# Kernel tuning notes

Hardware: AMD Instinct MI355X
Metric: run time of the kernel (lower is better)

The kernel has to match this reference:

```python
import jax, jax.numpy as jnp
import numpy as np

NUM_HEADS = 16


def setup_inputs() -> dict:
    key = jax.random.key(0)
    ks = jax.random.split(key, 6)
    B, N, L, C = 2, 1024, 4096, 1024
    x_obj = jax.random.normal(ks[0], (B, N, C), dtype=jnp.float32)
    x_ctx = jax.random.normal(ks[1], (B, L, C), dtype=jnp.float32)
    s = 1.0 / np.sqrt(C)
    Wq = jax.random.normal(ks[2], (C, C), dtype=jnp.float32) * s
    Wkv = jax.random.normal(ks[3], (C, 2 * C), dtype=jnp.float32) * s
    Wproj = jax.random.normal(ks[4], (C, C), dtype=jnp.float32) * s
    bproj = jax.random.normal(ks[5], (C,), dtype=jnp.float32) * 0.01
    return {"x_obj": x_obj, "x_ctx": x_ctx, "Wq": Wq, "Wkv": Wkv,
            "Wproj": Wproj, "bproj": bproj}


def _split_heads(t, H):
    # [B, T, C] -> [B, H, T, d]
    B, T, C = t.shape
    return t.reshape(B, T, H, C // H).transpose(0, 2, 1, 3)


def reference(x_obj, x_ctx, Wq, Wkv, Wproj, bproj):
    B, N, C = x_obj.shape
    H = NUM_HEADS
    d = C // H
    scale = d ** -0.5

    q = _split_heads(x_obj @ Wq, H)                      # [B,H,N,d]

    kv_o = x_obj @ Wkv                                   # [B,N,2C] -> (2,H,d) split
    k_obj = _split_heads(kv_o[..., :C], H)               # [B,H,N,d]
    v_obj = _split_heads(kv_o[..., C:], H)

    kv_c = x_ctx @ Wkv                                   # [B,L,2C]
    k_ctx = _split_heads(kv_c[..., :C], H)               # [B,H,L,d]
    v_ctx = _split_heads(kv_c[..., C:], H)

    k = jnp.concatenate([k_obj, k_ctx], axis=2)          # [B,H,N+L,d]
    v = jnp.concatenate([v_obj, v_ctx], axis=2)

    attn = jnp.einsum('bhnd,bhmd->bhnm', q, k) * scale   # [B,H,N,N+L]
    attn = jax.nn.softmax(attn, axis=-1)
    out = jnp.einsum('bhnm,bhmd->bhnd', attn, v)         # [B,H,N,d]
    out = out.transpose(0, 2, 1, 3).reshape(B, N, C)
    return out @ Wproj + bproj
```

## Files before the change

### kernel.cpp

```cpp
#include <hip/hip_runtime.h>
#include <stdint.h>

typedef unsigned short u16;
typedef unsigned int   u32;
typedef __attribute__((ext_vector_type(8))) short bf16x8;
typedef __attribute__((ext_vector_type(4))) float f32x4;

__device__ __forceinline__ u16 f2bf(float f) {
    union { float f; u32 u; } v; v.f = f;
    return (u16)((v.u + 0x7FFFu + ((v.u >> 16) & 1u)) >> 16);
}
__device__ __forceinline__ float bf2f(u16 h) {
    union { u32 u; float f; } v; v.u = ((u32)h) << 16; return v.f;
}
__device__ __forceinline__ u32 fbits(float f) {
    union { float f; u32 u; } v; v.f = f; return v.u;
}

__device__ __forceinline__ void async16(const u16* g, u16* l) {
    typedef __attribute__((address_space(1))) const u32 gq;
    typedef __attribute__((address_space(3))) u32 lq;
    __builtin_amdgcn_global_load_lds((gq*)g, (lq*)l, 16, 0, 0);
}

__global__ void cvt_all_k(const float* __restrict__ xo, const float* __restrict__ xc,
                          u16* __restrict__ Xc,
                          const float* __restrict__ Wq, const float* __restrict__ Wkv,
                          const float* __restrict__ Wp,
                          u16* __restrict__ Wqt, u16* __restrict__ Wkt,
                          u16* __restrict__ Wpt)
{
    __shared__ __align__(16) u16 Ts[64][72];
    int id = blockIdx.x, t = threadIdx.x;
    if (id < 10240) {
        int row = id, cid = t * 4;
        int b = row >= 5120, s = row - b * 5120;
        const float* src = (s < 1024)
            ? xo + ((size_t)(b * 1024 + s)) * 1024 + cid
            : xc + ((size_t)(b * 4096 + s - 1024)) * 1024 + cid;
        float4 f = *(const float4*)src;
        union { u16 a[4]; uint2 v; } p;
        p.a[0]=f2bf(f.x); p.a[1]=f2bf(f.y); p.a[2]=f2bf(f.z); p.a[3]=f2bf(f.w);
        *(uint2*)(Xc + (size_t)row * 1024 + cid) = p.v;
        return;
    }
    int wid = id - 10240;
    const float* W; u16* Wt; int N, tile;
    if (wid < 256)      { W = Wq;  Wt = Wqt; N = 1024; tile = wid; }
    else if (wid < 768) { W = Wkv; Wt = Wkt; N = 2048; tile = wid - 256; }
    else                { W = Wp;  Wt = Wpt; N = 1024; tile = wid - 768; }
    int nt = N >> 6;
    int n0 = (tile % nt) * 64, k0 = (tile / nt) * 64;
    int lr = t >> 2, lc = (t & 3) * 16;
    const float* src = W + (size_t)(k0 + lr) * N + n0 + lc;
    union { u16 a[8]; uint4 v; } p0, p1;
    float4 f0 = *(const float4*)(src),      f1 = *(const float4*)(src + 4);
    float4 f2 = *(const float4*)(src + 8),  f3 = *(const float4*)(src + 12);
    p0.a[0]=f2bf(f0.x); p0.a[1]=f2bf(f0.y); p0.a[2]=f2bf(f0.z); p0.a[3]=f2bf(f0.w);
    p0.a[4]=f2bf(f1.x); p0.a[5]=f2bf(f1.y); p0.a[6]=f2bf(f1.z); p0.a[7]=f2bf(f1.w);
    p1.a[0]=f2bf(f2.x); p1.a[1]=f2bf(f2.y); p1.a[2]=f2bf(f2.z); p1.a[3]=f2bf(f2.w);
    p1.a[4]=f2bf(f3.x); p1.a[5]=f2bf(f3.y); p1.a[6]=f2bf(f3.z); p1.a[7]=f2bf(f3.w);
    *(uint4*)&Ts[lr][lc]     = p0.v;
    *(uint4*)&Ts[lr][lc + 8] = p1.v;
    __syncthreads();
    union { u16 a[8]; uint4 v; } q0, q1;
#pragma unroll
    for (int j = 0; j < 8; ++j) q0.a[j] = Ts[lc + j][lr];
#pragma unroll
    for (int j = 0; j < 8; ++j) q1.a[j] = Ts[lc + 8 + j][lr];
    u16* dst = Wt + (size_t)(n0 + lr) * 1024 + k0 + lc;
    *(uint4*)dst       = q0.v;
    *(uint4*)(dst + 8) = q1.v;
}

__global__ __launch_bounds__(256, 2)
void gemm_qkv(const u16* __restrict__ A, const u16* __restrict__ Wqt,
              const u16* __restrict__ Wkt, u16* __restrict__ q,
              u16* __restrict__ Kh, u16* __restrict__ Vh)
{
    __shared__ __align__(16) u16 smem[17408];
    u16* As = smem;
    u16* Bs = smem + 4096;

    const int t = threadIdx.x, w = t >> 6;
    const int lane = t & 63, quad = lane >> 4, l16 = lane & 15;
    const int id = blockIdx.x;
    const bool qm = id >= 1280;
    int m0, n0; const u16* Bt;
    if (qm) { int t2 = id - 1280; m0 = (t2 >> 3) * 128; n0 = (t2 & 7) * 128; Bt = Wqt; }
    else    { m0 = (id >> 4) * 128; n0 = (id & 15) * 128; Bt = Wkt; }
    const int wr = (w >> 1) * 64, wc = (w & 1) * 64;

    const int sr0 = w * 32 + (lane >> 2), sr1 = sr0 + 16;
    const int cg  = (lane & 3) ^ ((lane >> 4) & 3);
    u16* abase = As + w * 1024;
    u16* bbase = Bs + w * 1024;

    const u16 *ar0, *ar1;
    {
        int g0 = m0 + sr0, g1 = m0 + sr1;
        if (qm) {
            ar0 = A + ((size_t)(g0 >> 10) * 5120 + (g0 & 1023)) * 1024;
            ar1 = A + ((size_t)(g1 >> 10) * 5120 + (g1 & 1023)) * 1024;
        } else {
            ar0 = A + (size_t)g0 * 1024;
            ar1 = A + (size_t)g1 * 1024;
        }
        ar0 += cg * 8; ar1 += cg * 8;
    }
    const u16* br0 = Bt + (size_t)(n0 + sr0) * 1024 + cg * 8;
    const u16* br1 = Bt + (size_t)(n0 + sr1) * 1024 + cg * 8;

    f32x4 acc[4][4] = {};
    const int sel = (quad ^ (l16 >> 2)) * 8;

    for (int k0 = 0; k0 < 1024; k0 += 32) {
        async16(ar0 + k0, abase);
        async16(ar1 + k0, abase + 512);
        async16(br0 + k0, bbase);
        async16(br1 + k0, bbase + 512);
        __syncthreads();

        bf16x8 av[4], bv[4];
#pragma unroll
        for (int i = 0; i < 4; ++i)
            av[i] = *(const bf16x8*)&As[(wr + i * 16 + l16) * 32 + sel];
#pragma unroll
        for (int j = 0; j < 4; ++j)
            bv[j] = *(const bf16x8*)&Bs[(wc + j * 16 + l16) * 32 + sel];
#pragma unroll
        for (int i = 0; i < 4; ++i)
#pragma unroll
            for (int j = 0; j < 4; ++j)
                acc[i][j] = __builtin_amdgcn_mfma_f32_16x16x32_bf16(av[i], bv[j], acc[i][j], 0, 0, 0);
        __syncthreads();
    }

    if (qm) {
        const float SC = 0.180336880f;
#pragma unroll
        for (int j = 0; j < 4; ++j) {
            int col = n0 + wc + j * 16 + l16;
#pragma unroll
            for (int i = 0; i < 4; ++i) {
                int rowb = m0 + wr + i * 16 + quad * 4;
#pragma unroll
                for (int r = 0; r < 4; ++r)
                    q[(size_t)(rowb + r) * 1024 + col] = f2bf(acc[i][j][r] * SC);
            }
        }
        return;
    }
    int b = m0 >= 5120;
    int keyb = m0 - b * 5120;
    if (n0 < 1024) {
#pragma unroll
        for (int j = 0; j < 4; ++j) {
            int col = n0 + wc + j * 16 + l16;
#pragma unroll
            for (int i = 0; i < 4; ++i) {
                int rowb = m0 + wr + i * 16 + quad * 4;
                int key = rowb - b * 5120;
                int bh = b * 16 + (col >> 6), d = col & 63;
                u16* dst = Kh + ((size_t)bh * 5120 + key) * 64 + d;
#pragma unroll
                for (int r = 0; r < 4; ++r) dst[r * 64] = f2bf(acc[i][j][r]);
            }
        }
    } else {
        u16* T = smem;
#pragma unroll
        for (int j = 0; j < 4; ++j) {
            int d2 = wc + j * 16 + l16;
#pragma unroll
            for (int i = 0; i < 4; ++i) {
                int kl = wr + i * 16 + quad * 4;
                union { u16 a[4]; uint2 v; } pk;
#pragma unroll
                for (int r = 0; r < 4; ++r) pk.a[r] = f2bf(acc[i][j][r]);
                *(uint2*)&T[d2 * 136 + kl] = pk.v;
            }
        }
        __syncthreads();
        int hb = (n0 - 1024) >> 6;
#pragma unroll
        for (int p = 0; p < 8; ++p) {
            int idx = p * 256 + t;
            int d2 = idx >> 4, k0c = (idx & 15) * 8;
            uint4 vv = *(const uint4*)&T[d2 * 136 + k0c];
            int bh = b * 16 + hb + (d2 >> 6), d = d2 & 63;
            *(uint4*)(Vh + ((size_t)bh * 64 + d) * 5120 + keyb + k0c) = vv;
        }
    }
}

__global__ __launch_bounds__(256, 2)
void gemm_proj(const u16* __restrict__ A, const u16* __restrict__ Bt,
               const float* __restrict__ bias, float* __restrict__ Cf)
{
    __shared__ __align__(16) u16 As[128 * 32];
    __shared__ __align__(16) u16 Bs[64 * 32];

    const int t = threadIdx.x, w = t >> 6;
    const int lane = t & 63, quad = lane >> 4, l16 = lane & 15;
    const int m0 = blockIdx.y * 128, n0 = blockIdx.x * 64;
    const int wr = w * 32;

    const int sr0 = w * 32 + (lane >> 2), sr1 = sr0 + 16;
    const int cg  = (lane & 3) ^ ((lane >> 4) & 3);
    u16* abase = As + w * 1024;
    u16* bbase = Bs + w * 512;

    const u16* ar0 = A + (size_t)(m0 + sr0) * 1024 + cg * 8;
    const u16* ar1 = A + (size_t)(m0 + sr1) * 1024 + cg * 8;
    const u16* br0 = Bt + (size_t)(n0 + w * 16 + (lane >> 2)) * 1024 + cg * 8;

    f32x4 acc[2][4] = {};
    const int sel = (quad ^ (l16 >> 2)) * 8;

    for (int k0 = 0; k0 < 1024; k0 += 32) {
        async16(ar0 + k0, abase);
        async16(ar1 + k0, abase + 512);
        async16(br0 + k0, bbase);
        __syncthreads();

        bf16x8 av[2], bv[4];
#pragma unroll
        for (int i = 0; i < 2; ++i)
            av[i] = *(const bf16x8*)&As[(wr + i * 16 + l16) * 32 + sel];
#pragma unroll
        for (int j = 0; j < 4; ++j)
            bv[j] = *(const bf16x8*)&Bs[(j * 16 + l16) * 32 + sel];
#pragma unroll
        for (int i = 0; i < 2; ++i)
#pragma unroll
            for (int j = 0; j < 4; ++j)
                acc[i][j] = __builtin_amdgcn_mfma_f32_16x16x32_bf16(av[i], bv[j], acc[i][j], 0, 0, 0);
        __syncthreads();
    }

#pragma unroll
    for (int j = 0; j < 4; ++j) {
        int col = n0 + j * 16 + l16;
        float bvl = bias[col];
#pragma unroll
        for (int i = 0; i < 2; ++i) {
            int rowb = m0 + wr + i * 16 + quad * 4;
#pragma unroll
            for (int r = 0; r < 4; ++r)
                Cf[(size_t)(rowb + r) * 1024 + col] = acc[i][j][r] + bvl;
        }
    }
}

__global__ __launch_bounds__(256, 4)
void attn_k(const u16* __restrict__ Q, const u16* __restrict__ Kh,
            const u16* __restrict__ Vh, u16* __restrict__ Op,
            float* __restrict__ Lp)
{
    __shared__ __align__(16) u16 Ks[2][4096];
    __shared__ __align__(16) u16 Vt[2][4096];
    __shared__ __align__(16) u16 Ps[4096];

    const int tid  = threadIdx.x;
    const int wave = tid >> 6, lane = tid & 63;
    const int quad = lane >> 4, l16 = lane & 15;
    const int bx = blockIdx.x;
    const int x   = bx & 7;
    const int seq = bx >> 3;
    const int qt  = seq & 7;
    const int kg  = seq >> 3;
    const int g   = x + 8 * kg;
    const int part = g >> 5;
    const int bh   = g & 31;
    const int h = bh & 15, b = bh >> 4;

    const int qrow0 = b * 1024 + qt * 128 + wave * 32;
    const u16* qbase = Q + (size_t)qrow0 * 1024 + h * 64;

    bf16x8 aq[2][2];
#pragma unroll
    for (int rt = 0; rt < 2; ++rt) {
        aq[rt][0] = *(const bf16x8*)(qbase + (size_t)(rt * 16 + l16) * 1024 +      quad * 8);
        aq[rt][1] = *(const bf16x8*)(qbase + (size_t)(rt * 16 + l16) * 1024 + 32 + quad * 8);
    }

    union { u32 u[4]; bf16x8 v; } onesf;
#pragma unroll
    for (int i = 0; i < 4; ++i) onesf.u[i] = 0x3F803F80u;

    f32x4 o[2][4] = {};
    f32x4 lacc[2] = {};

    const u16* kbase = Kh + (size_t)bh * 5120 * 64;
    const u16* vbase = Vh + (size_t)bh * 64 * 5120;
    const int l7 = l16 & 7;
    u16* psw = Ps + wave * 1024;
    const int m_beg = part * 1280;

    const int r1 = tid >> 3;
    const int sl = tid & 7;
    const int xs = sl ^ (r1 & 7);
    const u16* kga = kbase + (size_t)(m_beg + 2 * r1) * 64 + xs * 8;
    const u16* vga = vbase + (size_t)r1 * 5120 + m_beg + xs * 8;
    u16* kldsw = &Ks[0][0] + wave * 512;
    u16* vldsw = &Vt[0][0] + wave * 512;

    async16(kga,              kldsw);
    async16(kga + 64,         kldsw + 2048);
    async16(vga,              vldsw);
    async16(vga + 32 * 5120,  vldsw + 2048);

    for (int c = 0; c < 20; ++c) {
        __syncthreads();

        if (c < 19) {
            const int nb = (c + 1) & 1;
            const u16* ka = kga + (size_t)(c + 1) * 4096;
            const u16* va = vga + (c + 1) * 64;
            u16* kd = &Ks[nb][0] + wave * 512;
            u16* vd = &Vt[nb][0] + wave * 512;
            async16(ka,             kd);
            async16(ka + 64,        kd + 2048);
            async16(va,             vd);
            async16(va + 32 * 5120, vd + 2048);
        }

        const u16* KsC = &Ks[c & 1][0];
        const u16* VtC = &Vt[c & 1][0];

        f32x4 s[2][4] = {};
        __builtin_amdgcn_s_setprio(1);
#pragma unroll
        for (int nt = 0; nt < 4; ++nt) {
            const u16* krow = KsC + (nt * 16 + l16) * 64;
            bf16x8 kb0 = *(const bf16x8*)(krow + ((quad     ^ l7) * 8));
            bf16x8 kb1 = *(const bf16x8*)(krow + (((4+quad) ^ l7) * 8));
#pragma unroll
            for (int rt = 0; rt < 2; ++rt) {
                s[rt][nt] = __builtin_amdgcn_mfma_f32_16x16x32_bf16(aq[rt][0], kb0, s[rt][nt], 0, 0, 0);
                s[rt][nt] = __builtin_amdgcn_mfma_f32_16x16x32_bf16(aq[rt][1], kb1, s[rt][nt], 0, 0, 0);
            }
        }
        __builtin_amdgcn_s_setprio(0);

#pragma unroll
        for (int rt = 0; rt < 2; ++rt) {
#pragma unroll
            for (int r = 0; r < 4; ++r) {
                float e0 = exp2f(s[rt][0][r]);
                float e1 = exp2f(s[rt][1][r]);
                float e2 = exp2f(s[rt][2][r]);
                float e3 = exp2f(s[rt][3][r]);
                u32 pwx = __builtin_amdgcn_perm(fbits(e2), fbits(e0), 0x07060302u);
                u32 pwy = __builtin_amdgcn_perm(fbits(e3), fbits(e1), 0x07060302u);
                int qr = quad * 4 + r;
                u16* prow = psw + qr * 64;
                *(u32*)(prow + ((( (l16 >> 2)    ) ^ (qr & 7)) * 8) + (l16 & 3) * 2) = pwx;
                *(u32*)(prow + ((( (l16 >> 2) + 4) ^ (qr & 7)) * 8) + (l16 & 3) * 2) = pwy;
            }

            asm volatile("s_waitcnt lgkmcnt(0)" ::: "memory");

            const u16* prow = psw + l16 * 64;
            bf16x8 pf0 = *(const bf16x8*)(prow + ((quad     ^ l7) * 8));
            bf16x8 pf1 = *(const bf16x8*)(prow + (((4+quad) ^ l7) * 8));

            __builtin_amdgcn_s_setprio(1);
            lacc[rt] = __builtin_amdgcn_mfma_f32_16x16x32_bf16(pf0, onesf.v, lacc[rt], 0, 0, 0);
            lacc[rt] = __builtin_amdgcn_mfma_f32_16x16x32_bf16(pf1, onesf.v, lacc[rt], 0, 0, 0);
#pragma unroll
            for (int dt = 0; dt < 4; ++dt) {
                const u16* vrow = VtC + (dt * 16 + l16) * 64;
                bf16x8 v0 = *(const bf16x8*)(vrow + ((quad     ^ l7) * 8));
                bf16x8 v1 = *(const bf16x8*)(vrow + (((4+quad) ^ l7) * 8));
                o[rt][dt] = __builtin_amdgcn_mfma_f32_16x16x32_bf16(pf0, v0, o[rt][dt], 0, 0, 0);
                o[rt][dt] = __builtin_amdgcn_mfma_f32_16x16x32_bf16(pf1, v1, o[rt][dt], 0, 0, 0);
            }
            __builtin_amdgcn_s_setprio(0);
        }
    }

    const int Rb = bh * 1024 + qt * 128 + wave * 32;
    u16* obase = Op + ((size_t)part << 21);
#pragma unroll
    for (int rt = 0; rt < 2; ++rt)
#pragma unroll
        for (int dt = 0; dt < 4; ++dt)
#pragma unroll
            for (int r = 0; r < 4; ++r) {
                int R = Rb + rt * 16 + quad * 4 + r;
                obase[(size_t)R * 64 + dt * 16 + l16] = f2bf(o[rt][dt][r]);
            }
    if (l16 == 0) {
#pragma unroll
        for (int rt = 0; rt < 2; ++rt)
#pragma unroll
            for (int r = 0; r < 4; ++r)
                Lp[part * 32768 + Rb + rt * 16 + quad * 4 + r] = lacc[rt][r];
    }
}

__global__ void comb_k(const u16* __restrict__ Op, const float* __restrict__ Lp,
                       u16* __restrict__ ao)
{
    int t = blockIdx.x * 256 + threadIdx.x;
    int R = t >> 4, dg = (t & 15) * 4;
    float l = Lp[R] + Lp[32768 + R] + Lp[65536 + R] + Lp[98304 + R];
    float a[4] = {0.f, 0.f, 0.f, 0.f};
#pragma unroll
    for (int p = 0; p < 4; ++p) {
        union { u16 a[4]; uint2 v; } w;
        w.v = *(const uint2*)(Op + ((size_t)p << 21) + (size_t)R * 64 + dg);
#pragma unroll
        for (int j = 0; j < 4; ++j) a[j] += bf2f(w.a[j]);
    }
    float inv = 1.f / l;
    int bh = R >> 10, n = R & 1023, b = bh >> 4, h = bh & 15;
    union { u16 a[4]; uint2 v; } out;
#pragma unroll
    for (int j = 0; j < 4; ++j) out.a[j] = f2bf(a[j] * inv);
    *(uint2*)(ao + (size_t)(b * 1024 + n) * 1024 + h * 64 + dg) = out.v;
}

extern "C" void kernel_launch(void* const* d_in, const int* in_sizes, int n_in,
                              void* d_out, int out_size, void* d_ws, size_t ws_size,
                              hipStream_t stream)
{
    const float* x_obj = (const float*)d_in[0];
    const float* x_ctx = (const float*)d_in[1];
    const float* Wq    = (const float*)d_in[2];
    const float* Wkv   = (const float*)d_in[3];
    const float* Wproj = (const float*)d_in[4];
    const float* bproj = (const float*)d_in[5];
    float* out = (float*)d_out;

    u16* Xc  = (u16*)d_ws;
    u16* ao  = Xc;
    u16* Op  = Xc + (size_t)2097152;
    u16* Wqt = Xc  + (size_t)10485760;
    u16* Wkt = Wqt + (size_t)1048576;
    u16* Wpt = Wkt + (size_t)2097152;
    u16* q   = Wpt + (size_t)1048576;
    u16* Kh  = q   + (size_t)2097152;
    u16* Vh  = Kh  + (size_t)10485760;
    float* Lp = (float*)(Wkt + (size_t)1048576);

    dim3 blk(256);
    cvt_all_k<<<dim3(11264), blk, 0, stream>>>(x_obj, x_ctx, Xc,
                                               Wq, Wkv, Wproj, Wqt, Wkt, Wpt);
    gemm_qkv<<<dim3(1408), blk, 0, stream>>>(Xc, Wqt, Wkt, q, Kh, Vh);
    attn_k<<<dim3(1024), blk, 0, stream>>>(q, Kh, Vh, Op, Lp);
    comb_k<<<dim3(2048), blk, 0, stream>>>(Op, Lp, ao);
    gemm_proj<<<dim3(16, 16), blk, 0, stream>>>(ao, Wpt, bproj, out);
}
```

Before: 244.4 us.

## Hoist V fragments, software-pipeline P tiles, and stagger block start with sleeps

The inner attention loop now loads the V fragments once per chunk and shares them across both row tiles, where before they were reloaded for each row tile. The exponentials for the second row tile are computed while the first tile's P is staged through LDS, so exp work overlaps LDS traffic. The goal is to cut redundant LDS reads and hide latency between the exp and MFMA phases. It also adds a per-block s_sleep delay based on block index to stagger block start times. That spreads out contention at launch but inserts idle cycles, and the hoisted V fragments raise register pressure.

```diff
diff --git a/kernel.cpp b/kernel.cpp
--- a/kernel.cpp
+++ b/kernel.cpp
@@ -275,6 +275,14 @@
     const int bh   = g & 31;
     const int h = bh & 15, b = bh >> 4;
 
+    {
+        int ph = (bx >> 8) & 3;
+        for (int i = 0; i < ph; ++i) {
+            __builtin_amdgcn_s_sleep(8);
+            __builtin_amdgcn_s_sleep(8);
+        }
+    }
+
     const int qrow0 = b * 1024 + qt * 128 + wave * 32;
     const u16* qbase = Q + (size_t)qrow0 * 1024 + h * 64;
 
@@ -344,41 +352,77 @@
         }
         __builtin_amdgcn_s_setprio(0);
 
-#pragma unroll
-        for (int rt = 0; rt < 2; ++rt) {
-#pragma unroll
-            for (int r = 0; r < 4; ++r) {
-                float e0 = exp2f(s[rt][0][r]);
-                float e1 = exp2f(s[rt][1][r]);
-                float e2 = exp2f(s[rt][2][r]);
-                float e3 = exp2f(s[rt][3][r]);
-                u32 pwx = __builtin_amdgcn_perm(fbits(e2), fbits(e0), 0x07060302u);
-                u32 pwy = __builtin_amdgcn_perm(fbits(e3), fbits(e1), 0x07060302u);
-                int qr = quad * 4 + r;
-                u16* prow = psw + qr * 64;
-                *(u32*)(prow + ((( (l16 >> 2)    ) ^ (qr & 7)) * 8) + (l16 & 3) * 2) = pwx;
-                *(u32*)(prow + ((( (l16 >> 2) + 4) ^ (qr & 7)) * 8) + (l16 & 3) * 2) = pwy;
-            }
-
-            asm volatile("s_waitcnt lgkmcnt(0)" ::: "memory");
-
-            const u16* prow = psw + l16 * 64;
-            bf16x8 pf0 = *(const bf16x8*)(prow + ((quad     ^ l7) * 8));
-            bf16x8 pf1 = *(const bf16x8*)(prow + (((4+quad) ^ l7) * 8));
-
-            __builtin_amdgcn_s_setprio(1);
-            lacc[rt] = __builtin_amdgcn_mfma_f32_16x16x32_bf16(pf0, onesf.v, lacc[rt], 0, 0, 0);
-            lacc[rt] = __builtin_amdgcn_mfma_f32_16x16x32_bf16(pf1, onesf.v, lacc[rt], 0, 0, 0);
-#pragma unroll
-            for (int dt = 0; dt < 4; ++dt) {
-                const u16* vrow = VtC + (dt * 16 + l16) * 64;
-                bf16x8 v0 = *(const bf16x8*)(vrow + ((quad     ^ l7) * 8));
-                bf16x8 v1 = *(const bf16x8*)(vrow + (((4+quad) ^ l7) * 8));
-                o[rt][dt] = __builtin_amdgcn_mfma_f32_16x16x32_bf16(pf0, v0, o[rt][dt], 0, 0, 0);
-                o[rt][dt] = __builtin_amdgcn_mfma_f32_16x16x32_bf16(pf1, v1, o[rt][dt], 0, 0, 0);
-            }
-            __builtin_amdgcn_s_setprio(0);
-        }
+        bf16x8 vf0[4], vf1[4];
+#pragma unroll
+        for (int dt = 0; dt < 4; ++dt) {
+            const u16* vrow = VtC + (dt * 16 + l16) * 64;
+            vf0[dt] = *(const bf16x8*)(vrow + ((quad     ^ l7) * 8));
+            vf1[dt] = *(const bf16x8*)(vrow + (((4+quad) ^ l7) * 8));
+        }
+
+#pragma unroll
+        for (int r = 0; r < 4; ++r) {
+            float e0 = exp2f(s[0][0][r]);
+            float e1 = exp2f(s[0][1][r]);
+            float e2 = exp2f(s[0][2][r]);
+            float e3 = exp2f(s[0][3][r]);
+            u32 pwx = __builtin_amdgcn_perm(fbits(e2), fbits(e0), 0x07060302u);
+            u32 pwy = __builtin_amdgcn_perm(fbits(e3), fbits(e1), 0x07060302u);
+            int qr = quad * 4 + r;
+            u16* prow = psw + qr * 64;
+            *(u32*)(prow + ((( (l16 >> 2)    ) ^ (qr & 7)) * 8) + (l16 & 3) * 2) = pwx;
+            *(u32*)(prow + ((( (l16 >> 2) + 4) ^ (qr & 7)) * 8) + (l16 & 3) * 2) = pwy;
+        }
+
+        u32 pw1[4][2];
+#pragma unroll
+        for (int r = 0; r < 4; ++r) {
+            float e0 = exp2f(s[1][0][r]);
+            float e1 = exp2f(s[1][1][r]);
+            float e2 = exp2f(s[1][2][r]);
+            float e3 = exp2f(s[1][3][r]);
+            pw1[r][0] = __builtin_amdgcn_perm(fbits(e2), fbits(e0), 0x07060302u);
+            pw1[r][1] = __builtin_amdgcn_perm(fbits(e3), fbits(e1), 0x07060302u);
+        }
+
+        asm volatile("s_waitcnt lgkmcnt(0)" ::: "memory");
+
+        const u16* prow = psw + l16 * 64;
+        bf16x8 pf0a = *(const bf16x8*)(prow + ((quad     ^ l7) * 8));
+        bf16x8 pf0b = *(const bf16x8*)(prow + (((4+quad) ^ l7) * 8));
+
+#pragma unroll
+        for (int r = 0; r < 4; ++r) {
+            int qr = quad * 4 + r;
+            u16* prw = psw + qr * 64;
+            *(u32*)(prw + ((( (l16 >> 2)    ) ^ (qr & 7)) * 8) + (l16 & 3) * 2) = pw1[r][0];
+            *(u32*)(prw + ((( (l16 >> 2) + 4) ^ (qr & 7)) * 8) + (l16 & 3) * 2) = pw1[r][1];
+        }
+
+        __builtin_amdgcn_s_setprio(1);
+        lacc[0] = __builtin_amdgcn_mfma_f32_16x16x32_bf16(pf0a, onesf.v, lacc[0], 0, 0, 0);
+        lacc[0] = __builtin_amdgcn_mfma_f32_16x16x32_bf16(pf0b, onesf.v, lacc[0], 0, 0, 0);
+#pragma unroll
+        for (int dt = 0; dt < 4; ++dt) {
+            o[0][dt] = __builtin_amdgcn_mfma_f32_16x16x32_bf16(pf0a, vf0[dt], o[0][dt], 0, 0, 0);
+            o[0][dt] = __builtin_amdgcn_mfma_f32_16x16x32_bf16(pf0b, vf1[dt], o[0][dt], 0, 0, 0);
+        }
+        __builtin_amdgcn_s_setprio(0);
+
+        asm volatile("s_waitcnt lgkmcnt(0)" ::: "memory");
+
+        bf16x8 pf1a = *(const bf16x8*)(prow + ((quad     ^ l7) * 8));
+        bf16x8 pf1b = *(const bf16x8*)(prow + (((4+quad) ^ l7) * 8));
+
+        __builtin_amdgcn_s_setprio(1);
+        lacc[1] = __builtin_amdgcn_mfma_f32_16x16x32_bf16(pf1a, onesf.v, lacc[1], 0, 0, 0);
+        lacc[1] = __builtin_amdgcn_mfma_f32_16x16x32_bf16(pf1b, onesf.v, lacc[1], 0, 0, 0);
+#pragma unroll
+        for (int dt = 0; dt < 4; ++dt) {
+            o[1][dt] = __builtin_amdgcn_mfma_f32_16x16x32_bf16(pf1a, vf0[dt], o[1][dt], 0, 0, 0);
+            o[1][dt] = __builtin_amdgcn_mfma_f32_16x16x32_bf16(pf1b, vf1[dt], o[1][dt], 0, 0, 0);
+        }
+        __builtin_amdgcn_s_setprio(0);
     }
 
     const int Rb = bh * 1024 + qt * 128 + wave * 32;
```

After: 270.4 us. 10.7% more time.

## Keep softmax probabilities in registers by transposing QK MFMA and permuting V

Applied to the files above, without the earlier changes.

The QK^T MFMA operands are swapped so the score fragment comes out transposed. Each lane can then pack its exp values straight into the A-operand layout for the PV MFMA, which removes the per-wave LDS round trip for P, its waitcnt stall and the Ps shared buffer. To match the new column order, V is loaded through registers with a permuted key offset and written into LDS itself, replacing the async global-to-LDS copy. K rows are now loaded contiguously instead of interleaved. The cost is more VGPR pressure and register-staged V loads that the asynchronous copy path no longer hides.

```diff
diff --git a/kernel.cpp b/kernel.cpp
--- a/kernel.cpp
+++ b/kernel.cpp
@@ -260,7 +260,6 @@
 {
     __shared__ __align__(16) u16 Ks[2][4096];
     __shared__ __align__(16) u16 Vt[2][4096];
-    __shared__ __align__(16) u16 Ps[4096];
 
     const int tid  = threadIdx.x;
     const int wave = tid >> 6, lane = tid & 63;
@@ -295,35 +294,48 @@
     const u16* kbase = Kh + (size_t)bh * 5120 * 64;
     const u16* vbase = Vh + (size_t)bh * 64 * 5120;
     const int l7 = l16 & 7;
-    u16* psw = Ps + wave * 1024;
     const int m_beg = part * 1280;
 
     const int r1 = tid >> 3;
     const int sl = tid & 7;
     const int xs = sl ^ (r1 & 7);
-    const u16* kga = kbase + (size_t)(m_beg + 2 * r1) * 64 + xs * 8;
-    const u16* vga = vbase + (size_t)r1 * 5120 + m_beg + xs * 8;
+    const u16* kga = kbase + (size_t)(m_beg + r1) * 64 + xs * 8;
     u16* kldsw = &Ks[0][0] + wave * 512;
-    u16* vldsw = &Vt[0][0] + wave * 512;
-
-    async16(kga,              kldsw);
-    async16(kga + 64,         kldsw + 2048);
-    async16(vga,              vldsw);
-    async16(vga + 32 * 5120,  vldsw + 2048);
+    const int koff = (xs < 4) ? (xs * 4) : (32 + (xs - 4) * 4);
+    const u16* vga0 = vbase + (size_t)r1 * 5120 + m_beg + koff;
+    const u16* vga1 = vga0 + (size_t)32 * 5120;
+    u16* vd0 = (u16*)0;
+    const int vdoff0 = r1 * 64 + sl * 8;
+    const int vdoff1 = (32 + r1) * 64 + sl * 8;
+
+    async16(kga,        kldsw);
+    async16(kga + 2048, kldsw + 2048);
+    uint2 va0 = *(const uint2*)(vga0);
+    uint2 va1 = *(const uint2*)(vga0 + 16);
+    uint2 vb0 = *(const uint2*)(vga1);
+    uint2 vb1 = *(const uint2*)(vga1 + 16);
 
     for (int c = 0; c < 20; ++c) {
+        {
+            u16* vbuf = &Vt[c & 1][0];
+            uint4 w0; w0.x = va0.x; w0.y = va0.y; w0.z = va1.x; w0.w = va1.y;
+            uint4 w1; w1.x = vb0.x; w1.y = vb0.y; w1.z = vb1.x; w1.w = vb1.y;
+            *(uint4*)(vbuf + vdoff0) = w0;
+            *(uint4*)(vbuf + vdoff1) = w1;
+        }
         __syncthreads();
 
         if (c < 19) {
-            const int nb = (c + 1) & 1;
             const u16* ka = kga + (size_t)(c + 1) * 4096;
-            const u16* va = vga + (c + 1) * 64;
-            u16* kd = &Ks[nb][0] + wave * 512;
-            u16* vd = &Vt[nb][0] + wave * 512;
-            async16(ka,             kd);
-            async16(ka + 64,        kd + 2048);
-            async16(va,             vd);
-            async16(va + 32 * 5120, vd + 2048);
+            u16* kd = &Ks[(c + 1) & 1][0] + wave * 512;
+            async16(ka,        kd);
+            async16(ka + 2048, kd + 2048);
+            const u16* vp0 = vga0 + (c + 1) * 64;
+            const u16* vp1 = vga1 + (c + 1) * 64;
+            va0 = *(const uint2*)(vp0);
+            va1 = *(const uint2*)(vp0 + 16);
+            vb0 = *(const uint2*)(vp1);
+            vb1 = *(const uint2*)(vp1 + 16);
         }
 
         const u16* KsC = &Ks[c & 1][0];
@@ -338,47 +350,44 @@
             bf16x8 kb1 = *(const bf16x8*)(krow + (((4+quad) ^ l7) * 8));
 #pragma unroll
             for (int rt = 0; rt < 2; ++rt) {
-                s[rt][nt] = __builtin_amdgcn_mfma_f32_16x16x32_bf16(aq[rt][0], kb0, s[rt][nt], 0, 0, 0);
-                s[rt][nt] = __builtin_amdgcn_mfma_f32_16x16x32_bf16(aq[rt][1], kb1, s[rt][nt], 0, 0, 0);
+                s[rt][nt] = __builtin_amdgcn_mfma_f32_16x16x32_bf16(kb0, aq[rt][0], s[rt][nt], 0, 0, 0);
+                s[rt][nt] = __builtin_amdgcn_mfma_f32_16x16x32_bf16(kb1, aq[rt][1], s[rt][nt], 0, 0, 0);
             }
         }
         __builtin_amdgcn_s_setprio(0);
 
+        union { u32 u[4]; bf16x8 v; } pa[2][2];
+#pragma unroll
+        for (int rt = 0; rt < 2; ++rt)
+#pragma unroll
+            for (int hf = 0; hf < 2; ++hf)
+#pragma unroll
+                for (int m = 0; m < 4; ++m) {
+                    int nt = 2 * hf + (m >> 1);
+                    int re = 2 * (m & 1);
+                    float ee = exp2f(s[rt][nt][re]);
+                    float eo = exp2f(s[rt][nt][re + 1]);
+                    pa[rt][hf].u[m] = __builtin_amdgcn_perm(fbits(eo), fbits(ee), 0x07060302u);
+                }
+
+        __builtin_amdgcn_s_setprio(1);
 #pragma unroll
         for (int rt = 0; rt < 2; ++rt) {
-#pragma unroll
-            for (int r = 0; r < 4; ++r) {
-                float e0 = exp2f(s[rt][0][r]);
-                float e1 = exp2f(s[rt][1][r]);
-                float e2 = exp2f(s[rt][2][r]);
-                float e3 = exp2f(s[rt][3][r]);
-                u32 pwx = __builtin_amdgcn_perm(fbits(e2), fbits(e0), 0x07060302u);
-                u32 pwy = __builtin_amdgcn_perm(fbits(e3), fbits(e1), 0x07060302u);
-                int qr = quad * 4 + r;
-                u16* prow = psw + qr * 64;
-                *(u32*)(prow + ((( (l16 >> 2)    ) ^ (qr & 7)) * 8) + (l16 & 3) * 2) = pwx;
-                *(u32*)(prow + ((( (l16 >> 2) + 4) ^ (qr & 7)) * 8) + (l16 & 3) * 2) = pwy;
-            }
-
-            asm volatile("s_waitcnt lgkmcnt(0)" ::: "memory");
-
-            const u16* prow = psw + l16 * 64;
-            bf16x8 pf0 = *(const bf16x8*)(prow + ((quad     ^ l7) * 8));
-            bf16x8 pf1 = *(const bf16x8*)(prow + (((4+quad) ^ l7) * 8));
-
-            __builtin_amdgcn_s_setprio(1);
-            lacc[rt] = __builtin_amdgcn_mfma_f32_16x16x32_bf16(pf0, onesf.v, lacc[rt], 0, 0, 0);
-            lacc[rt] = __builtin_amdgcn_mfma_f32_16x16x32_bf16(pf1, onesf.v, lacc[rt], 0, 0, 0);
-#pragma unroll
-            for (int dt = 0; dt < 4; ++dt) {
-                const u16* vrow = VtC + (dt * 16 + l16) * 64;
-                bf16x8 v0 = *(const bf16x8*)(vrow + ((quad     ^ l7) * 8));
-                bf16x8 v1 = *(const bf16x8*)(vrow + (((4+quad) ^ l7) * 8));
-                o[rt][dt] = __builtin_amdgcn_mfma_f32_16x16x32_bf16(pf0, v0, o[rt][dt], 0, 0, 0);
-                o[rt][dt] = __builtin_amdgcn_mfma_f32_16x16x32_bf16(pf1, v1, o[rt][dt], 0, 0, 0);
-            }
-            __builtin_amdgcn_s_setprio(0);
-        }
+            lacc[rt] = __builtin_amdgcn_mfma_f32_16x16x32_bf16(pa[rt][0].v, onesf.v, lacc[rt], 0, 0, 0);
+            lacc[rt] = __builtin_amdgcn_mfma_f32_16x16x32_bf16(pa[rt][1].v, onesf.v, lacc[rt], 0, 0, 0);
+        }
+#pragma unroll
+        for (int dt = 0; dt < 4; ++dt) {
+            const u16* vrow = VtC + (dt * 16 + l16) * 64;
+            bf16x8 v0 = *(const bf16x8*)(vrow + ((quad     ^ l7) * 8));
+            bf16x8 v1 = *(const bf16x8*)(vrow + (((4+quad) ^ l7) * 8));
+#pragma unroll
+            for (int rt = 0; rt < 2; ++rt) {
+                o[rt][dt] = __builtin_amdgcn_mfma_f32_16x16x32_bf16(pa[rt][0].v, v0, o[rt][dt], 0, 0, 0);
+                o[rt][dt] = __builtin_amdgcn_mfma_f32_16x16x32_bf16(pa[rt][1].v, v1, o[rt][dt], 0, 0, 0);
+            }
+        }
+        __builtin_amdgcn_s_setprio(0);
     }
 
     const int Rb = bh * 1024 + qt * 128 + wave * 32;
```

Measured after the change: 247.3 us. No clear change (+1.2%).
